# Kernel optimization log

Measured on AMD Instinct MI355X. Metric: run time of the kernel, lower is better.

Reference implementation:

```python
import jax, jax.numpy as jnp
import numpy as np

B, S, E = 4, 2048, 1024
H, DK, DV = 16, 64, 128


def setup_inputs() -> dict:
    key = jax.random.key(0)
    ks = jax.random.split(key, 9)
    scale = 0.02
    x = jax.random.normal(ks[0], (B, S, E), dtype=jnp.float32)
    # Per-head linear weights stacked along a head axis (same math as the
    # torch ModuleList of nn.Linear(embed_dim, d) layers).
    Wq = jax.random.normal(ks[1], (H, E, DK), dtype=jnp.float32) * scale
    bq = jax.random.normal(ks[2], (H, DK), dtype=jnp.float32) * scale
    Wk = jax.random.normal(ks[3], (H, E, DK), dtype=jnp.float32) * scale
    bk = jax.random.normal(ks[4], (H, DK), dtype=jnp.float32) * scale
    Wv = jax.random.normal(ks[5], (H, E, DV), dtype=jnp.float32) * scale
    bv = jax.random.normal(ks[6], (H, DV), dtype=jnp.float32) * scale
    Wo = jax.random.normal(ks[7], (H * DV, E), dtype=jnp.float32) * scale
    bo = jax.random.normal(ks[8], (E,), dtype=jnp.float32) * scale
    return {"x": x, "Wq": Wq, "bq": bq, "Wk": Wk, "bk": bk,
            "Wv": Wv, "bv": bv, "Wo": Wo, "bo": bo}


def reference(x, Wq, bq, Wk, bk, Wv, bv, Wo, bo):
    # Batched equivalent of the per-head Linear loop: [B,S,E] x [H,E,D] -> [B,H,S,D]
    Q = jnp.einsum('bse,hed->bhsd', x, Wq) + bq[None, :, None, :]
    K = jnp.einsum('bse,hed->bhsd', x, Wk) + bk[None, :, None, :]
    V = jnp.einsum('bse,hed->bhsd', x, Wv) + bv[None, :, None, :]
    scale = 1.0 / jnp.sqrt(jnp.asarray(Q.shape[-1], dtype=Q.dtype))
    scores = jnp.einsum('bhqd,bhkd->bhqk', Q, K) * scale  # [B,H,S,S]
    causal_mask = jnp.triu(jnp.ones((S, S), dtype=bool), k=1)  # True above diagonal
    scores = jnp.where(causal_mask[None, None], jnp.asarray(-jnp.inf, scores.dtype), scores)
    probs = jax.nn.softmax(scores, axis=-1)
    attn = jnp.einsum('bhqk,bhkd->bhqd', probs, V)  # [B,H,S,DV]
    # transpose(1,2).view(B,S,H*DV)
    concat = attn.transpose(0, 2, 1, 3).reshape(x.shape[0], x.shape[1], -1)
    return concat @ Wo + bo
```

## Files before the change

kernel.cpp:

```cpp
#include <hip/hip_runtime.h>

typedef __bf16 bf16x8 __attribute__((ext_vector_type(8)));
typedef float f32x4 __attribute__((ext_vector_type(4)));
typedef float f32x16 __attribute__((ext_vector_type(16)));

static constexpr int Bb = 4, Ss = 2048, Ee = 1024, Hh = 16, DKk = 64, DVv = 128;
static constexpr int Mm = Bb * Ss;
static constexpr int NQ = Hh * DKk;
static constexpr int NV = Hh * DVv;

#define MFMA16 __builtin_amdgcn_mfma_f32_16x16x32_bf16
#define MFMA32 __builtin_amdgcn_mfma_f32_32x32x16_bf16

#define GLL16(g, l) __builtin_amdgcn_global_load_lds(                        \
    (const __attribute__((address_space(1))) void*)(g),                      \
    (__attribute__((address_space(3))) void*)(l), 16, 0, 0)

#define SBAR()   asm volatile("s_barrier" ::: "memory")
#define WLGKM0() do { asm volatile("s_waitcnt lgkmcnt(0)" ::: "memory"); \
                      __builtin_amdgcn_sched_barrier(0); } while (0)
#define WVM(n)   asm volatile("s_waitcnt vmcnt(" #n ")" ::: "memory")

static __device__ __forceinline__ unsigned short f2b(float f) {
  unsigned int u = __float_as_uint(f);
  u += 0x7fffu + ((u >> 16) & 1u);
  return (unsigned short)(u >> 16);
}

__global__ __launch_bounds__(256) void cast_x_kernel(const float* __restrict__ in,
                                                     unsigned short* __restrict__ out, int n4) {
  int i = blockIdx.x * 256 + threadIdx.x;
  if (i >= n4) return;
  float4 v = reinterpret_cast<const float4*>(in)[i];
  ushort4 o;
  o.x = f2b(v.x); o.y = f2b(v.y); o.z = f2b(v.z); o.w = f2b(v.w);
  reinterpret_cast<ushort4*>(out)[i] = o;
}

__global__ __launch_bounds__(256) void transpose_cast_kernel(const float* __restrict__ in,
                                                             unsigned short* __restrict__ out,
                                                             int R, int C) {
  __shared__ float tile[32][33];
  int c0 = blockIdx.x * 32, r0 = blockIdx.y * 32;
  const float* ip = in + (size_t)blockIdx.z * R * C;
  unsigned short* op = out + (size_t)blockIdx.z * R * C;
  int tx = threadIdx.x, ty = threadIdx.y;
#pragma unroll
  for (int i = 0; i < 32; i += 8)
    tile[ty + i][tx] = ip[(size_t)(r0 + ty + i) * C + (c0 + tx)];
  __syncthreads();
#pragma unroll
  for (int i = 0; i < 32; i += 8)
    op[(size_t)(c0 + ty + i) * R + (r0 + tx)] = f2b(tile[tx][ty + i]);
}

template <int OUTMODE>
__global__ __launch_bounds__(512, 2) void gemm9_kernel(const unsigned short* __restrict__ A,
                                                       const unsigned short* __restrict__ BT,
                                                       const float* __restrict__ bias1,
                                                       const float* __restrict__ bias2,
                                                       void* __restrict__ out1,
                                                       void* __restrict__ out2,
                                                       int N, int K) {
  __shared__ unsigned short As0[256 * 64], As1[256 * 64];
  __shared__ unsigned short Bs0[256 * 64], Bs1[256 * 64];
  const int tid = threadIdx.x, wave = tid >> 6, lane = tid & 63;
  const int wm = wave >> 2, wn = wave & 3;
  const int l15 = lane & 15, lq = lane >> 4;
  const int nwg = gridDim.x, cpx = nwg >> 3;
  const int orig = (blockIdx.x & 7) * cpx + (blockIdx.x >> 3);
  const int bm = (orig & 31) << 8, bn = (orig >> 5) << 8;
  const int srow = tid >> 3;
  const int ssw = (((tid & 7) ^ (srow & 7)) << 3);
  const int rsw = l15 & 7;
  const int nIter = K >> 7;

  f32x4 acc[8][4] = {};
  bf16x8 bf[2][4];

#define LDA9(ASQ, MI, KK) \
  (*reinterpret_cast<const bf16x8*>(&(ASQ)[(size_t)((wm * 128 + (MI)*16 + l15) * 64) + (((((KK)*4 + lq)) ^ rsw) << 3)]))
#define LDB9(BSQ, NI, KK) \
  (*reinterpret_cast<const bf16x8*>(&(BSQ)[(size_t)((wn * 64 + (NI)*16 + l15) * 64) + (((((KK)*4 + lq)) ^ rsw) << 3)]))

  auto stA = [&](unsigned short* dst, int kt) {
#pragma unroll
    for (int k4 = 0; k4 < 4; ++k4)
      GLL16(A + (size_t)(bm + srow + k4 * 64) * K + kt * 64 + ssw,
            &dst[(size_t)(tid + k4 * 512) * 8]);
  };
  auto stB = [&](unsigned short* dst, int kt) {
#pragma unroll
    for (int k4 = 0; k4 < 4; ++k4)
      GLL16(BT + (size_t)(bn + srow + k4 * 64) * K + kt * 64 + ssw,
            &dst[(size_t)(tid + k4 * 512) * 8]);
  };

  stA(As0, 0);
  stB(Bs0, 0);
  stB(Bs1, 1);
  WVM(0);
  SBAR();

  for (int it = 0; it < nIter; ++it) {
    const bool notlast = (it < nIter - 1);
    {
      bf16x8 af[2][4];
#pragma unroll
      for (int kk = 0; kk < 2; ++kk)
#pragma unroll
        for (int m = 0; m < 4; ++m) af[kk][m] = LDA9(As0, m, kk);
#pragma unroll
      for (int kk = 0; kk < 2; ++kk)
#pragma unroll
        for (int ni = 0; ni < 4; ++ni) bf[kk][ni] = LDB9(Bs0, ni, kk);
      stA(As1, 2 * it + 1);
      SBAR();
      WLGKM0();
      __builtin_amdgcn_s_setprio(1);
#pragma unroll
      for (int kk = 0; kk < 2; ++kk)
#pragma unroll
        for (int m = 0; m < 4; ++m)
#pragma unroll
          for (int ni = 0; ni < 4; ++ni)
            acc[m][ni] = MFMA16(af[kk][m], bf[kk][ni], acc[m][ni], 0, 0, 0);
      __builtin_amdgcn_s_setprio(0);
      SBAR();
    }
    {
      bf16x8 af[2][4];
#pragma unroll
      for (int kk = 0; kk < 2; ++kk)
#pragma unroll
        for (int m = 0; m < 4; ++m) af[kk][m] = LDA9(As0, 4 + m, kk);
      if (notlast) stB(Bs0, 2 * it + 2);
      SBAR();
      WLGKM0();
      __builtin_amdgcn_s_setprio(1);
#pragma unroll
      for (int kk = 0; kk < 2; ++kk)
#pragma unroll
        for (int m = 0; m < 4; ++m)
#pragma unroll
          for (int ni = 0; ni < 4; ++ni)
            acc[4 + m][ni] = MFMA16(af[kk][m], bf[kk][ni], acc[4 + m][ni], 0, 0, 0);
      __builtin_amdgcn_s_setprio(0);
      if (notlast) { WVM(4); } else { WVM(0); }
      SBAR();
    }
    {
      bf16x8 af[2][4];
#pragma unroll
      for (int kk = 0; kk < 2; ++kk)
#pragma unroll
        for (int m = 0; m < 4; ++m) af[kk][m] = LDA9(As1, m, kk);
#pragma unroll
      for (int kk = 0; kk < 2; ++kk)
#pragma unroll
        for (int ni = 0; ni < 4; ++ni) bf[kk][ni] = LDB9(Bs1, ni, kk);
      if (notlast) stA(As0, 2 * it + 2);
      SBAR();
      WLGKM0();
      __builtin_amdgcn_s_setprio(1);
#pragma unroll
      for (int kk = 0; kk < 2; ++kk)
#pragma unroll
        for (int m = 0; m < 4; ++m)
#pragma unroll
          for (int ni = 0; ni < 4; ++ni)
            acc[m][ni] = MFMA16(af[kk][m], bf[kk][ni], acc[m][ni], 0, 0, 0);
      __builtin_amdgcn_s_setprio(0);
      SBAR();
    }
    {
      bf16x8 af[2][4];
#pragma unroll
      for (int kk = 0; kk < 2; ++kk)
#pragma unroll
        for (int m = 0; m < 4; ++m) af[kk][m] = LDA9(As1, 4 + m, kk);
      if (notlast) stB(Bs1, 2 * it + 3);
      SBAR();
      WLGKM0();
      __builtin_amdgcn_s_setprio(1);
#pragma unroll
      for (int kk = 0; kk < 2; ++kk)
#pragma unroll
        for (int m = 0; m < 4; ++m)
#pragma unroll
          for (int ni = 0; ni < 4; ++ni)
            acc[4 + m][ni] = MFMA16(af[kk][m], bf[kk][ni], acc[4 + m][ni], 0, 0, 0);
      __builtin_amdgcn_s_setprio(0);
      if (notlast) WVM(4);
      SBAR();
    }
  }

  const float SCLQ = 0.125f * 1.44269504088896f;
#pragma unroll
  for (int ni = 0; ni < 4; ++ni) {
    int col = bn + wn * 64 + ni * 16 + l15;
    float bs;
    if (OUTMODE == 4)
      bs = (col < 1024) ? bias1[col] : bias2[col - 1024];
    else
      bs = bias1[col];
#pragma unroll
    for (int mi = 0; mi < 8; ++mi) {
      int row0 = bm + wm * 128 + mi * 16 + (lq << 2);
      if (OUTMODE == 2) {
        int b_ = row0 >> 11, s0 = row0 & 2047;
        unsigned short* dst = (unsigned short*)out1 +
            ((size_t)((b_ * Hh + (col >> 7)) * DVv + (col & 127))) * Ss + s0;
        ushort4 o;
        o.x = f2b(acc[mi][ni][0] + bs);
        o.y = f2b(acc[mi][ni][1] + bs);
        o.z = f2b(acc[mi][ni][2] + bs);
        o.w = f2b(acc[mi][ni][3] + bs);
        *reinterpret_cast<ushort4*>(dst) = o;
      } else {
        unsigned short* tgt = (unsigned short*)(col < 1024 ? out1 : out2);
        int cc = col & 1023, hh = cc >> 6, d = cc & 63;
#pragma unroll
        for (int r = 0; r < 4; ++r) {
          int row = row0 + r;
          int b_ = row >> 11, s0 = row & 2047;
          float v = acc[mi][ni][r] + bs;
          if (col < 1024) v *= SCLQ;
          tgt[(((size_t)(b_ * Hh + hh) * Ss + s0) << 6) + d] = f2b(v);
        }
      }
    }
  }
#undef LDA9
#undef LDB9
}

__global__ __launch_bounds__(512, 2) void gemm8f_kernel(const unsigned short* __restrict__ A,
                                                        const unsigned short* __restrict__ BT,
                                                        const float* __restrict__ bias1,
                                                        float* __restrict__ out1,
                                                        int N, int K) {
  __shared__ unsigned short As0[256 * 64], As1[256 * 64];
  __shared__ unsigned short Bs0[128 * 64], Bs1[128 * 64];
  const int tid = threadIdx.x, wave = tid >> 6, lane = tid & 63;
  const int wm = wave >> 1, wn = wave & 1;
  const int l15 = lane & 15, lq = lane >> 4;
  const int nwg = gridDim.x, cpx = nwg >> 3;
  const int orig = (blockIdx.x & 7) * cpx + (blockIdx.x >> 3);
  const int bm = (orig & 31) << 8, bn = (orig >> 5) << 7;
  const int srow = tid >> 3;
  const int ssw = (((tid & 7) ^ (srow & 7)) << 3);
  const int rsw = l15 & 7;
  const int nIter = K >> 7;

  f32x4 acc[4][4] = {};
  bf16x8 bf[2][4];

#define LDA(ASQ, MI, KK) \
  (*reinterpret_cast<const bf16x8*>(&(ASQ)[(size_t)((wm * 64 + (MI)*16 + l15) * 64) + (((((KK)*4 + lq)) ^ rsw) << 3)]))
#define LDB(BSQ, NI, KK) \
  (*reinterpret_cast<const bf16x8*>(&(BSQ)[(size_t)((wn * 64 + (NI)*16 + l15) * 64) + (((((KK)*4 + lq)) ^ rsw) << 3)]))

  auto stA = [&](unsigned short* dst, int kt) {
#pragma unroll
    for (int k4 = 0; k4 < 4; ++k4)
      GLL16(A + (size_t)(bm + srow + k4 * 64) * K + kt * 64 + ssw,
            &dst[(size_t)(tid + k4 * 512) * 8]);
  };
  auto stB = [&](unsigned short* dst, int kt) {
#pragma unroll
    for (int k4 = 0; k4 < 2; ++k4)
      GLL16(BT + (size_t)(bn + srow + k4 * 64) * K + kt * 64 + ssw,
            &dst[(size_t)(tid + k4 * 512) * 8]);
  };

  stA(As0, 0);
  stB(Bs0, 0);
  stB(Bs1, 1);
  WVM(0);
  SBAR();

  for (int it = 0; it < nIter; ++it) {
    const bool notlast = (it < nIter - 1);
    {
      bf16x8 af[2][2];
      af[0][0] = LDA(As0, 0, 0); af[0][1] = LDA(As0, 1, 0);
      af[1][0] = LDA(As0, 0, 1); af[1][1] = LDA(As0, 1, 1);
#pragma unroll
      for (int kk = 0; kk < 2; ++kk)
#pragma unroll
        for (int ni = 0; ni < 4; ++ni) bf[kk][ni] = LDB(Bs0, ni, kk);
      stA(As1, 2 * it + 1);
      SBAR();
      WLGKM0();
      __builtin_amdgcn_s_setprio(1);
#pragma unroll
      for (int kk = 0; kk < 2; ++kk)
#pragma unroll
        for (int i = 0; i < 2; ++i)
#pragma unroll
          for (int ni = 0; ni < 4; ++ni)
            acc[i][ni] = MFMA16(af[kk][i], bf[kk][ni], acc[i][ni], 0, 0, 0);
      __builtin_amdgcn_s_setprio(0);
      SBAR();
    }
    {
      bf16x8 af[2][2];
      af[0][0] = LDA(As0, 2, 0); af[0][1] = LDA(As0, 3, 0);
      af[1][0] = LDA(As0, 2, 1); af[1][1] = LDA(As0, 3, 1);
      if (notlast) stB(Bs0, 2 * it + 2);
      SBAR();
      WLGKM0();
      __builtin_amdgcn_s_setprio(1);
#pragma unroll
      for (int kk = 0; kk < 2; ++kk)
#pragma unroll
        for (int i = 0; i < 2; ++i)
#pragma unroll
          for (int ni = 0; ni < 4; ++ni)
            acc[2 + i][ni] = MFMA16(af[kk][i], bf[kk][ni], acc[2 + i][ni], 0, 0, 0);
      __builtin_amdgcn_s_setprio(0);
      if (notlast) { WVM(2); } else { WVM(0); }
      SBAR();
    }
    {
      bf16x8 af[2][2];
      af[0][0] = LDA(As1, 0, 0); af[0][1] = LDA(As1, 1, 0);
      af[1][0] = LDA(As1, 0, 1); af[1][1] = LDA(As1, 1, 1);
#pragma unroll
      for (int kk = 0; kk < 2; ++kk)
#pragma unroll
        for (int ni = 0; ni < 4; ++ni) bf[kk][ni] = LDB(Bs1, ni, kk);
      if (notlast) stA(As0, 2 * it + 2);
      SBAR();
      WLGKM0();
      __builtin_amdgcn_s_setprio(1);
#pragma unroll
      for (int kk = 0; kk < 2; ++kk)
#pragma unroll
        for (int i = 0; i < 2; ++i)
#pragma unroll
          for (int ni = 0; ni < 4; ++ni)
            acc[i][ni] = MFMA16(af[kk][i], bf[kk][ni], acc[i][ni], 0, 0, 0);
      __builtin_amdgcn_s_setprio(0);
      SBAR();
    }
    {
      bf16x8 af[2][2];
      af[0][0] = LDA(As1, 2, 0); af[0][1] = LDA(As1, 3, 0);
      af[1][0] = LDA(As1, 2, 1); af[1][1] = LDA(As1, 3, 1);
      if (notlast) stB(Bs1, 2 * it + 3);
      SBAR();
      WLGKM0();
      __builtin_amdgcn_s_setprio(1);
#pragma unroll
      for (int kk = 0; kk < 2; ++kk)
#pragma unroll
        for (int i = 0; i < 2; ++i)
#pragma unroll
          for (int ni = 0; ni < 4; ++ni)
            acc[2 + i][ni] = MFMA16(af[kk][i], bf[kk][ni], acc[2 + i][ni], 0, 0, 0);
      __builtin_amdgcn_s_setprio(0);
      if (notlast) WVM(2);
      SBAR();
    }
  }

#pragma unroll
  for (int ni = 0; ni < 4; ++ni) {
    int col = bn + wn * 64 + ni * 16 + l15;
    float bs = bias1[col];
#pragma unroll
    for (int mi = 0; mi < 4; ++mi) {
      int row0 = bm + wm * 64 + mi * 16 + (lq << 2);
#pragma unroll
      for (int r = 0; r < 4; ++r)
        out1[(size_t)(row0 + r) * N + col] = acc[mi][ni][r] + bs;
    }
  }
#undef LDA
#undef LDB
}

__global__ __launch_bounds__(512, 1) void attn14_kernel(const unsigned short* __restrict__ Qh,
                                                        const unsigned short* __restrict__ Kh,
                                                        const unsigned short* __restrict__ Vt,
                                                        unsigned short* __restrict__ Aw) {
  __shared__ unsigned short Kb[2][128 * 64];
  __shared__ unsigned short Vb[2][128 * 128];
  const int bid = blockIdx.x;
  const int xcd = bid & 7, sub_ = bid >> 3;
  const int bhL = sub_ >> 2, q = sub_ & 3;
  const int bh = xcd + (bhL << 3);
  const int b = bh >> 4, h = bh & 15;
  const int tid = threadIdx.x, wave = tid >> 6, lane = tid & 63;
  const int l31 = lane & 31, lh = lane >> 5;

  const unsigned short* Qsrc = Qh + (size_t)(b * Hh + h) * Ss * DKk;
  const unsigned short* Ksrc = Kh + (size_t)(b * Hh + h) * Ss * DKk;
  const unsigned short* Vsrc = Vt + (size_t)(b * Hh + h) * (size_t)DVv * Ss;
  unsigned short* Adst = Aw + (size_t)b * Ss * NV + h * DVv;

  const int srowK = tid >> 3, schK = tid & 7;
  const int srowV = tid >> 4, schV = tid & 15;
  const int rx = l31 & 7;
  const int rxv = l31 & 15;

  union PU { unsigned u[4]; bf16x8 v; };

#pragma unroll 1
  for (int ph = 0; ph < 2; ++ph) {
    const int qt = ph ? q : 7 - q;
    const int nt2 = (qt + 1) * 2;
    const int q0w = qt * 256 + wave * 32;

    bf16x8 qf[4];
#pragma unroll
    for (int ks = 0; ks < 4; ++ks)
      qf[ks] = *reinterpret_cast<const bf16x8*>(
          Qsrc + (size_t)(q0w + l31) * DKk + ks * 16 + lh * 8);

    f32x16 accO[4] = {};
    float mrow = -1e30f, lrow = 0.f;

    {
#pragma unroll
      for (int k4 = 0; k4 < 2; ++k4) {
        int kvr = srowK + k4 * 64;
        GLL16(Ksrc + (size_t)kvr * DKk + ((schK ^ (kvr & 7)) << 3),
              &Kb[0][(size_t)(tid + k4 * 512) * 8]);
      }
#pragma unroll
      for (int k4 = 0; k4 < 4; ++k4) {
        int dvr = srowV + k4 * 32;
        GLL16(Vsrc + (size_t)dvr * Ss + ((schV ^ (dvr & 15)) << 3),
              &Vb[0][(size_t)(tid + k4 * 512) * 8]);
      }
    }

    for (int T = 0; T < nt2; ++T) {
      const int cur = T & 1;
      __syncthreads();
      if (T + 1 < nt2) {
        const int nb2 = (T + 1) * 128;
        const int nxt = cur ^ 1;
#pragma unroll
        for (int k4 = 0; k4 < 2; ++k4) {
          int kvr = srowK + k4 * 64;
          GLL16(Ksrc + (size_t)(nb2 + kvr) * DKk + ((schK ^ (kvr & 7)) << 3),
                &Kb[nxt][(size_t)(tid + k4 * 512) * 8]);
        }
#pragma unroll
        for (int k4 = 0; k4 < 4; ++k4) {
          int dvr = srowV + k4 * 32;
          GLL16(Vsrc + (size_t)dvr * Ss + nb2 + ((schV ^ (dvr & 15)) << 3),
                &Vb[nxt][(size_t)(tid + k4 * 512) * 8]);
        }
      }
#pragma unroll 1
      for (int sub = 0; sub < 2; ++sub) {
        const int kbase = T * 128 + sub * 64;
        if (kbase > q0w + 31) continue;

        f32x16 accS[2] = {};
        __builtin_amdgcn_s_setprio(1);
#pragma unroll
        for (int kvb = 0; kvb < 2; ++kvb)
#pragma unroll
          for (int ks = 0; ks < 4; ++ks) {
            const int row = sub * 64 + kvb * 32 + l31;
            bf16x8 kf = *reinterpret_cast<const bf16x8*>(
                &Kb[cur][row * 64 + (((ks * 2 + lh) ^ rx) << 3)]);
            accS[kvb] = MFMA32(kf, qf[ks], accS[kvb], 0, 0, 0);
          }
        __builtin_amdgcn_s_setprio(0);

        if (kbase + 63 > q0w) {
          int qg = q0w + l31;
#pragma unroll
          for (int kvb = 0; kvb < 2; ++kvb)
#pragma unroll
            for (int reg = 0; reg < 16; ++reg) {
              int kvg = kbase + kvb * 32 + (reg & 3) + 8 * (reg >> 2) + 4 * lh;
              if (kvg > qg) accS[kvb][reg] = -1e30f;
            }
        }
        float t[8];
#pragma unroll
        for (int i = 0; i < 8; ++i)
          t[i] = fmaxf(fmaxf(accS[0][i], accS[0][i + 8]), fmaxf(accS[1][i], accS[1][i + 8]));
        float pmx = fmaxf(fmaxf(fmaxf(t[0], t[1]), fmaxf(t[2], t[3])),
                          fmaxf(fmaxf(t[4], t[5]), fmaxf(t[6], t[7])));
        pmx = fmaxf(pmx, __shfl_xor(pmx, 32));
        float mn = mrow;
        if (!__all(pmx - mn <= 8.f)) {
          float mnew = fmaxf(mn, pmx);
          float al = exp2f(mn - mnew);
          mrow = mnew;
          lrow *= al;
#pragma unroll
          for (int reg = 0; reg < 16; ++reg) {
            float a = __shfl(al, (reg & 3) + 8 * (reg >> 2) + 4 * lh);
#pragma unroll
            for (int dvb = 0; dvb < 4; ++dvb) accO[dvb][reg] *= a;
          }
          mn = mnew;
        }
        float rs = 0.f;
#pragma unroll
        for (int kvb = 0; kvb < 2; ++kvb)
#pragma unroll
          for (int reg = 0; reg < 16; ++reg) {
            float e = exp2f(accS[kvb][reg] - mn);
            accS[kvb][reg] = e;
            rs += e;
          }
        rs += __shfl_xor(rs, 32);
        lrow += rs;
        bf16x8 pfrag[4];
#pragma unroll
        for (int kvb = 0; kvb < 2; ++kvb)
#pragma unroll
          for (int s = 0; s < 2; ++s) {
            const int B0 = s * 8;
            unsigned a, c, bb, d;
            asm("v_cvt_pk_bf16_f32 %0, %1, %2" : "=v"(a) : "v"(accS[kvb][B0 + 0]), "v"(accS[kvb][B0 + 1]));
            asm("v_cvt_pk_bf16_f32 %0, %1, %2" : "=v"(c) : "v"(accS[kvb][B0 + 2]), "v"(accS[kvb][B0 + 3]));
            asm("v_cvt_pk_bf16_f32 %0, %1, %2" : "=v"(bb) : "v"(accS[kvb][B0 + 4]), "v"(accS[kvb][B0 + 5]));
            asm("v_cvt_pk_bf16_f32 %0, %1, %2" : "=v"(d) : "v"(accS[kvb][B0 + 6]), "v"(accS[kvb][B0 + 7]));
            asm volatile("v_permlane32_swap_b32 %0, %1" : "+v"(a), "+v"(bb));
            asm volatile("v_permlane32_swap_b32 %0, %1" : "+v"(c), "+v"(d));
            PU u;
            u.u[0] = a; u.u[1] = c; u.u[2] = bb; u.u[3] = d;
            pfrag[kvb * 2 + s] = u.v;
          }
        __builtin_amdgcn_s_setprio(1);
#pragma unroll
        for (int dvb = 0; dvb < 4; ++dvb) {
          const int dv = dvb * 32 + l31;
          const unsigned short* vr = &Vb[cur][dv * 128];
#pragma unroll
          for (int ks = 0; ks < 4; ++ks) {
            bf16x8 vf = *reinterpret_cast<const bf16x8*>(
                vr + ((((sub << 3) + ks * 2 + lh) ^ rxv) << 3));
            accO[dvb] = MFMA32(pfrag[ks], vf, accO[dvb], 0, 0, 0);
          }
        }
        __builtin_amdgcn_s_setprio(0);
      }
    }
    float linv = 1.f / lrow;
#pragma unroll
    for (int reg = 0; reg < 16; ++reg) {
      int qr = (reg & 3) + 8 * (reg >> 2) + 4 * lh;
      float li = __shfl(linv, qr);
      int row = q0w + qr;
#pragma unroll
      for (int dvb = 0; dvb < 4; ++dvb)
        Adst[(size_t)row * NV + dvb * 32 + l31] = f2b(accO[dvb][reg] * li);
    }
    __syncthreads();
  }
}

extern "C" void kernel_launch(void* const* d_in, const int* in_sizes, int n_in,
                              void* d_out, int out_size, void* d_ws, size_t ws_size,
                              hipStream_t stream) {
  (void)in_sizes; (void)n_in; (void)out_size; (void)ws_size;
  const float* x  = (const float*)d_in[0];
  const float* Wq = (const float*)d_in[1];
  const float* bq = (const float*)d_in[2];
  const float* Wk = (const float*)d_in[3];
  const float* bk = (const float*)d_in[4];
  const float* Wv = (const float*)d_in[5];
  const float* bv = (const float*)d_in[6];
  const float* Wo = (const float*)d_in[7];
  const float* bo = (const float*)d_in[8];
  float* out = (float*)d_out;

  unsigned short* ws = (unsigned short*)d_ws;
  unsigned short* xb  = ws;
  unsigned short* WqT = xb  + 8388608;
  unsigned short* WkT = WqT + 1048576;
  unsigned short* WvT = WkT + 1048576;
  unsigned short* WoT = WvT + 2097152;
  unsigned short* Qw  = WoT + 2097152;
  unsigned short* Kw  = Qw  + 8388608;
  unsigned short* Vtw = Kw  + 8388608;
  unsigned short* Aw  = Vtw + 16777216;

  cast_x_kernel<<<dim3(8192), dim3(256), 0, stream>>>(x, xb, (Mm * Ee) / 4);

  transpose_cast_kernel<<<dim3(2, 32, 16), dim3(32, 8), 0, stream>>>(Wq, WqT, Ee, DKk);
  transpose_cast_kernel<<<dim3(2, 32, 16), dim3(32, 8), 0, stream>>>(Wk, WkT, Ee, DKk);
  transpose_cast_kernel<<<dim3(4, 32, 16), dim3(32, 8), 0, stream>>>(Wv, WvT, Ee, DVv);
  transpose_cast_kernel<<<dim3(32, 64, 1), dim3(32, 8), 0, stream>>>(Wo, WoT, NV, Ee);

  gemm9_kernel<4><<<dim3(256), dim3(512), 0, stream>>>(xb, WqT, bq, bk, Qw, Kw, 2048, Ee);
  gemm9_kernel<2><<<dim3(256), dim3(512), 0, stream>>>(xb, WvT, bv, nullptr, Vtw, nullptr, NV, Ee);

  attn14_kernel<<<dim3(256), dim3(512), 0, stream>>>(Qw, Kw, Vtw, Aw);

  gemm8f_kernel<<<dim3(256), dim3(512), 0, stream>>>(Aw, WoT, bo, out, NQ, NV);
}
```

Measured before the change: 246.6 us.

## Restructure GEMM mainloops into per-tile double-buffered prefetch; tree-reduce softmax row sums

```diff
diff --git a/kernel.cpp b/kernel.cpp
--- a/kernel.cpp
+++ b/kernel.cpp
@@ -55,13 +55,13 @@
 }
 
 template <int OUTMODE>
-__global__ __launch_bounds__(512, 2) void gemm9_kernel(const unsigned short* __restrict__ A,
-                                                       const unsigned short* __restrict__ BT,
-                                                       const float* __restrict__ bias1,
-                                                       const float* __restrict__ bias2,
-                                                       void* __restrict__ out1,
-                                                       void* __restrict__ out2,
-                                                       int N, int K) {
+__global__ __launch_bounds__(512, 2) void gemm10_kernel(const unsigned short* __restrict__ A,
+                                                        const unsigned short* __restrict__ BT,
+                                                        const float* __restrict__ bias1,
+                                                        const float* __restrict__ bias2,
+                                                        void* __restrict__ out1,
+                                                        void* __restrict__ out2,
+                                                        int N, int K) {
   __shared__ unsigned short As0[256 * 64], As1[256 * 64];
   __shared__ unsigned short Bs0[256 * 64], Bs1[256 * 64];
   const int tid = threadIdx.x, wave = tid >> 6, lane = tid & 63;
@@ -73,15 +73,14 @@
   const int srow = tid >> 3;
   const int ssw = (((tid & 7) ^ (srow & 7)) << 3);
   const int rsw = l15 & 7;
-  const int nIter = K >> 7;
+  const int nIter = K >> 6;
 
   f32x4 acc[8][4] = {};
-  bf16x8 bf[2][4];
-
-#define LDA9(ASQ, MI, KK) \
-  (*reinterpret_cast<const bf16x8*>(&(ASQ)[(size_t)((wm * 128 + (MI)*16 + l15) * 64) + (((((KK)*4 + lq)) ^ rsw) << 3)]))
-#define LDB9(BSQ, NI, KK) \
-  (*reinterpret_cast<const bf16x8*>(&(BSQ)[(size_t)((wn * 64 + (NI)*16 + l15) * 64) + (((((KK)*4 + lq)) ^ rsw) << 3)]))
+
+#define LDAx(P, MI, KK) \
+  (*reinterpret_cast<const bf16x8*>(&(P)[(size_t)((wm * 128 + (MI)*16 + l15) * 64) + (((((KK)*4 + lq)) ^ rsw) << 3)]))
+#define LDBx(P, NI, KK) \
+  (*reinterpret_cast<const bf16x8*>(&(P)[(size_t)((wn * 64 + (NI)*16 + l15) * 64) + (((((KK)*4 + lq)) ^ rsw) << 3)]))
 
   auto stA = [&](unsigned short* dst, int kt) {
 #pragma unroll
@@ -96,104 +95,58 @@
             &dst[(size_t)(tid + k4 * 512) * 8]);
   };
 
+  auto tile = [&](int t, unsigned short* Acur, unsigned short* Bcur,
+                  unsigned short* Anxt, unsigned short* Bnxt) {
+    SBAR();
+    if (t + 1 < nIter) {
+      stA(Anxt, t + 1);
+      stB(Bnxt, t + 1);
+      WVM(8);
+    } else {
+      WVM(0);
+    }
+    SBAR();
+    bf16x8 bfr[2][4], af[2][4];
+#pragma unroll
+    for (int kk = 0; kk < 2; ++kk)
+#pragma unroll
+      for (int ni = 0; ni < 4; ++ni) bfr[kk][ni] = LDBx(Bcur, ni, kk);
+#pragma unroll
+    for (int kk = 0; kk < 2; ++kk)
+#pragma unroll
+      for (int m = 0; m < 4; ++m) af[kk][m] = LDAx(Acur, m, kk);
+    WLGKM0();
+    __builtin_amdgcn_s_setprio(1);
+#pragma unroll
+    for (int kk = 0; kk < 2; ++kk)
+#pragma unroll
+      for (int m = 0; m < 4; ++m)
+#pragma unroll
+        for (int ni = 0; ni < 4; ++ni)
+          acc[m][ni] = MFMA16(af[kk][m], bfr[kk][ni], acc[m][ni], 0, 0, 0);
+    __builtin_amdgcn_s_setprio(0);
+#pragma unroll
+    for (int kk = 0; kk < 2; ++kk)
+#pragma unroll
+      for (int m = 0; m < 4; ++m) af[kk][m] = LDAx(Acur, 4 + m, kk);
+    WLGKM0();
+    __builtin_amdgcn_s_setprio(1);
+#pragma unroll
+    for (int kk = 0; kk < 2; ++kk)
+#pragma unroll
+      for (int m = 0; m < 4; ++m)
+#pragma unroll
+        for (int ni = 0; ni < 4; ++ni)
+          acc[4 + m][ni] = MFMA16(af[kk][m], bfr[kk][ni], acc[4 + m][ni], 0, 0, 0);
+    __builtin_amdgcn_s_setprio(0);
+  };
+
   stA(As0, 0);
   stB(Bs0, 0);
-  stB(Bs1, 1);
-  WVM(0);
-  SBAR();
-
-  for (int it = 0; it < nIter; ++it) {
-    const bool notlast = (it < nIter - 1);
-    {
-      bf16x8 af[2][4];
-#pragma unroll
-      for (int kk = 0; kk < 2; ++kk)
-#pragma unroll
-        for (int m = 0; m < 4; ++m) af[kk][m] = LDA9(As0, m, kk);
-#pragma unroll
-      for (int kk = 0; kk < 2; ++kk)
-#pragma unroll
-        for (int ni = 0; ni < 4; ++ni) bf[kk][ni] = LDB9(Bs0, ni, kk);
-      stA(As1, 2 * it + 1);
-      SBAR();
-      WLGKM0();
-      __builtin_amdgcn_s_setprio(1);
-#pragma unroll
-      for (int kk = 0; kk < 2; ++kk)
-#pragma unroll
-        for (int m = 0; m < 4; ++m)
-#pragma unroll
-          for (int ni = 0; ni < 4; ++ni)
-            acc[m][ni] = MFMA16(af[kk][m], bf[kk][ni], acc[m][ni], 0, 0, 0);
-      __builtin_amdgcn_s_setprio(0);
-      SBAR();
-    }
-    {
-      bf16x8 af[2][4];
-#pragma unroll
-      for (int kk = 0; kk < 2; ++kk)
-#pragma unroll
-        for (int m = 0; m < 4; ++m) af[kk][m] = LDA9(As0, 4 + m, kk);
-      if (notlast) stB(Bs0, 2 * it + 2);
-      SBAR();
-      WLGKM0();
-      __builtin_amdgcn_s_setprio(1);
-#pragma unroll
-      for (int kk = 0; kk < 2; ++kk)
-#pragma unroll
-        for (int m = 0; m < 4; ++m)
-#pragma unroll
-          for (int ni = 0; ni < 4; ++ni)
-            acc[4 + m][ni] = MFMA16(af[kk][m], bf[kk][ni], acc[4 + m][ni], 0, 0, 0);
-      __builtin_amdgcn_s_setprio(0);
-      if (notlast) { WVM(4); } else { WVM(0); }
-      SBAR();
-    }
-    {
-      bf16x8 af[2][4];
-#pragma unroll
-      for (int kk = 0; kk < 2; ++kk)
-#pragma unroll
-        for (int m = 0; m < 4; ++m) af[kk][m] = LDA9(As1, m, kk);
-#pragma unroll
-      for (int kk = 0; kk < 2; ++kk)
-#pragma unroll
-        for (int ni = 0; ni < 4; ++ni) bf[kk][ni] = LDB9(Bs1, ni, kk);
-      if (notlast) stA(As0, 2 * it + 2);
-      SBAR();
-      WLGKM0();
-      __builtin_amdgcn_s_setprio(1);
-#pragma unroll
-      for (int kk = 0; kk < 2; ++kk)
-#pragma unroll
-        for (int m = 0; m < 4; ++m)
-#pragma unroll
-          for (int ni = 0; ni < 4; ++ni)
-            acc[m][ni] = MFMA16(af[kk][m], bf[kk][ni], acc[m][ni], 0, 0, 0);
-      __builtin_amdgcn_s_setprio(0);
-      SBAR();
-    }
-    {
-      bf16x8 af[2][4];
-#pragma unroll
-      for (int kk = 0; kk < 2; ++kk)
-#pragma unroll
-        for (int m = 0; m < 4; ++m) af[kk][m] = LDA9(As1, 4 + m, kk);
-      if (notlast) stB(Bs1, 2 * it + 3);
-      SBAR();
-      WLGKM0();
-      __builtin_amdgcn_s_setprio(1);
-#pragma unroll
-      for (int kk = 0; kk < 2; ++kk)
-#pragma unroll
-        for (int m = 0; m < 4; ++m)
-#pragma unroll
-          for (int ni = 0; ni < 4; ++ni)
-            acc[4 + m][ni] = MFMA16(af[kk][m], bf[kk][ni], acc[4 + m][ni], 0, 0, 0);
-      __builtin_amdgcn_s_setprio(0);
-      if (notlast) WVM(4);
-      SBAR();
-    }
+
+  for (int it = 0; it < nIter; it += 2) {
+    tile(it, As0, Bs0, As1, Bs1);
+    tile(it + 1, As1, Bs1, As0, Bs0);
   }
 
   const float SCLQ = 0.125f * 1.44269504088896f;
@@ -232,15 +185,15 @@
       }
     }
   }
-#undef LDA9
-#undef LDB9
-}
-
-__global__ __launch_bounds__(512, 2) void gemm8f_kernel(const unsigned short* __restrict__ A,
-                                                        const unsigned short* __restrict__ BT,
-                                                        const float* __restrict__ bias1,
-                                                        float* __restrict__ out1,
-                                                        int N, int K) {
+#undef LDAx
+#undef LDBx
+}
+
+__global__ __launch_bounds__(512, 2) void gemm10f_kernel(const unsigned short* __restrict__ A,
+                                                         const unsigned short* __restrict__ BT,
+                                                         const float* __restrict__ bias1,
+                                                         float* __restrict__ out1,
+                                                         int N, int K) {
   __shared__ unsigned short As0[256 * 64], As1[256 * 64];
   __shared__ unsigned short Bs0[128 * 64], Bs1[128 * 64];
   const int tid = threadIdx.x, wave = tid >> 6, lane = tid & 63;
@@ -252,15 +205,14 @@
   const int srow = tid >> 3;
   const int ssw = (((tid & 7) ^ (srow & 7)) << 3);
   const int rsw = l15 & 7;
-  const int nIter = K >> 7;
+  const int nIter = K >> 6;
 
   f32x4 acc[4][4] = {};
-  bf16x8 bf[2][4];
-
-#define LDA(ASQ, MI, KK) \
-  (*reinterpret_cast<const bf16x8*>(&(ASQ)[(size_t)((wm * 64 + (MI)*16 + l15) * 64) + (((((KK)*4 + lq)) ^ rsw) << 3)]))
-#define LDB(BSQ, NI, KK) \
-  (*reinterpret_cast<const bf16x8*>(&(BSQ)[(size_t)((wn * 64 + (NI)*16 + l15) * 64) + (((((KK)*4 + lq)) ^ rsw) << 3)]))
+
+#define LDAf(P, MI, KK) \
+  (*reinterpret_cast<const bf16x8*>(&(P)[(size_t)((wm * 64 + (MI)*16 + l15) * 64) + (((((KK)*4 + lq)) ^ rsw) << 3)]))
+#define LDBf(P, NI, KK) \
+  (*reinterpret_cast<const bf16x8*>(&(P)[(size_t)((wn * 64 + (NI)*16 + l15) * 64) + (((((KK)*4 + lq)) ^ rsw) << 3)]))
 
   auto stA = [&](unsigned short* dst, int kt) {
 #pragma unroll
@@ -275,96 +227,44 @@
             &dst[(size_t)(tid + k4 * 512) * 8]);
   };
 
+  auto tile = [&](int t, unsigned short* Acur, unsigned short* Bcur,
+                  unsigned short* Anxt, unsigned short* Bnxt) {
+    SBAR();
+    if (t + 1 < nIter) {
+      stA(Anxt, t + 1);
+      stB(Bnxt, t + 1);
+      WVM(6);
+    } else {
+      WVM(0);
+    }
+    SBAR();
+    bf16x8 bfr[2][4], af[2][4];
+#pragma unroll
+    for (int kk = 0; kk < 2; ++kk)
+#pragma unroll
+      for (int ni = 0; ni < 4; ++ni) bfr[kk][ni] = LDBf(Bcur, ni, kk);
+#pragma unroll
+    for (int kk = 0; kk < 2; ++kk)
+#pragma unroll
+      for (int m = 0; m < 4; ++m) af[kk][m] = LDAf(Acur, m, kk);
+    WLGKM0();
+    __builtin_amdgcn_s_setprio(1);
+#pragma unroll
+    for (int kk = 0; kk < 2; ++kk)
+#pragma unroll
+      for (int m = 0; m < 4; ++m)
+#pragma unroll
+        for (int ni = 0; ni < 4; ++ni)
+          acc[m][ni] = MFMA16(af[kk][m], bfr[kk][ni], acc[m][ni], 0, 0, 0);
+    __builtin_amdgcn_s_setprio(0);
+  };
+
   stA(As0, 0);
   stB(Bs0, 0);
-  stB(Bs1, 1);
-  WVM(0);
-  SBAR();
-
-  for (int it = 0; it < nIter; ++it) {
-    const bool notlast = (it < nIter - 1);
-    {
-      bf16x8 af[2][2];
-      af[0][0] = LDA(As0, 0, 0); af[0][1] = LDA(As0, 1, 0);
-      af[1][0] = LDA(As0, 0, 1); af[1][1] = LDA(As0, 1, 1);
-#pragma unroll
-      for (int kk = 0; kk < 2; ++kk)
-#pragma unroll
-        for (int ni = 0; ni < 4; ++ni) bf[kk][ni] = LDB(Bs0, ni, kk);
-      stA(As1, 2 * it + 1);
-      SBAR();
-      WLGKM0();
-      __builtin_amdgcn_s_setprio(1);
-#pragma unroll
-      for (int kk = 0; kk < 2; ++kk)
-#pragma unroll
-        for (int i = 0; i < 2; ++i)
-#pragma unroll
-          for (int ni = 0; ni < 4; ++ni)
-            acc[i][ni] = MFMA16(af[kk][i], bf[kk][ni], acc[i][ni], 0, 0, 0);
-      __builtin_amdgcn_s_setprio(0);
-      SBAR();
-    }
-    {
-      bf16x8 af[2][2];
-      af[0][0] = LDA(As0, 2, 0); af[0][1] = LDA(As0, 3, 0);
-      af[1][0] = LDA(As0, 2, 1); af[1][1] = LDA(As0, 3, 1);
-      if (notlast) stB(Bs0, 2 * it + 2);
-      SBAR();
-      WLGKM0();
-      __builtin_amdgcn_s_setprio(1);
-#pragma unroll
-      for (int kk = 0; kk < 2; ++kk)
-#pragma unroll
-        for (int i = 0; i < 2; ++i)
-#pragma unroll
-          for (int ni = 0; ni < 4; ++ni)
-            acc[2 + i][ni] = MFMA16(af[kk][i], bf[kk][ni], acc[2 + i][ni], 0, 0, 0);
-      __builtin_amdgcn_s_setprio(0);
-      if (notlast) { WVM(2); } else { WVM(0); }
-      SBAR();
-    }
-    {
-      bf16x8 af[2][2];
-      af[0][0] = LDA(As1, 0, 0); af[0][1] = LDA(As1, 1, 0);
-      af[1][0] = LDA(As1, 0, 1); af[1][1] = LDA(As1, 1, 1);
-#pragma unroll
-      for (int kk = 0; kk < 2; ++kk)
-#pragma unroll
-        for (int ni = 0; ni < 4; ++ni) bf[kk][ni] = LDB(Bs1, ni, kk);
-      if (notlast) stA(As0, 2 * it + 2);
-      SBAR();
-      WLGKM0();
-      __builtin_amdgcn_s_setprio(1);
-#pragma unroll
-      for (int kk = 0; kk < 2; ++kk)
-#pragma unroll
-        for (int i = 0; i < 2; ++i)
-#pragma unroll
-          for (int ni = 0; ni < 4; ++ni)
-            acc[i][ni] = MFMA16(af[kk][i], bf[kk][ni], acc[i][ni], 0, 0, 0);
-      __builtin_amdgcn_s_setprio(0);
-      SBAR();
-    }
-    {
-      bf16x8 af[2][2];
-      af[0][0] = LDA(As1, 2, 0); af[0][1] = LDA(As1, 3, 0);
-      af[1][0] = LDA(As1, 2, 1); af[1][1] = LDA(As1, 3, 1);
-      if (notlast) stB(Bs1, 2 * it + 3);
-      SBAR();
-      WLGKM0();
-      __builtin_amdgcn_s_setprio(1);
-#pragma unroll
-      for (int kk = 0; kk < 2; ++kk)
-#pragma unroll
-        for (int i = 0; i < 2; ++i)
-#pragma unroll
-          for (int ni = 0; ni < 4; ++ni)
-            acc[2 + i][ni] = MFMA16(af[kk][i], bf[kk][ni], acc[2 + i][ni], 0, 0, 0);
-      __builtin_amdgcn_s_setprio(0);
-      if (notlast) WVM(2);
-      SBAR();
-    }
+
+  for (int it = 0; it < nIter; it += 2) {
+    tile(it, As0, Bs0, As1, Bs1);
+    tile(it + 1, As1, Bs1, As0, Bs0);
   }
 
 #pragma unroll
@@ -379,11 +279,11 @@
         out1[(size_t)(row0 + r) * N + col] = acc[mi][ni][r] + bs;
     }
   }
-#undef LDA
-#undef LDB
-}
-
-__global__ __launch_bounds__(512, 1) void attn14_kernel(const unsigned short* __restrict__ Qh,
+#undef LDAf
+#undef LDBf
+}
+
+__global__ __launch_bounds__(512, 1) void attn15_kernel(const unsigned short* __restrict__ Qh,
                                                         const unsigned short* __restrict__ Kh,
                                                         const unsigned short* __restrict__ Vt,
                                                         unsigned short* __restrict__ Aw) {
@@ -507,17 +407,22 @@
           }
           mn = mnew;
         }
-        float rs = 0.f;
 #pragma unroll
         for (int kvb = 0; kvb < 2; ++kvb)
 #pragma unroll
-          for (int reg = 0; reg < 16; ++reg) {
-            float e = exp2f(accS[kvb][reg] - mn);
-            accS[kvb][reg] = e;
-            rs += e;
-          }
-        rs += __shfl_xor(rs, 32);
-        lrow += rs;
+          for (int reg = 0; reg < 16; ++reg)
+            accS[kvb][reg] = exp2f(accS[kvb][reg] - mn);
+        {
+          f32x16 sv = accS[0] + accS[1];
+          float s8[8];
+#pragma unroll
+          for (int i = 0; i < 8; ++i) s8[i] = sv[i] + sv[i + 8];
+          float s40 = s8[0] + s8[4], s41 = s8[1] + s8[5];
+          float s42 = s8[2] + s8[6], s43 = s8[3] + s8[7];
+          float rs = (s40 + s41) + (s42 + s43);
+          rs += __shfl_xor(rs, 32);
+          lrow += rs;
+        }
         bf16x8 pfrag[4];
 #pragma unroll
         for (int kvb = 0; kvb < 2; ++kvb)
@@ -597,10 +502,10 @@
   transpose_cast_kernel<<<dim3(4, 32, 16), dim3(32, 8), 0, stream>>>(Wv, WvT, Ee, DVv);
   transpose_cast_kernel<<<dim3(32, 64, 1), dim3(32, 8), 0, stream>>>(Wo, WoT, NV, Ee);
 
-  gemm9_kernel<4><<<dim3(256), dim3(512), 0, stream>>>(xb, WqT, bq, bk, Qw, Kw, 2048, Ee);
-  gemm9_kernel<2><<<dim3(256), dim3(512), 0, stream>>>(xb, WvT, bv, nullptr, Vtw, nullptr, NV, Ee);
-
-  attn14_kernel<<<dim3(256), dim3(512), 0, stream>>>(Qw, Kw, Vtw, Aw);
-
-  gemm8f_kernel<<<dim3(256), dim3(512), 0, stream>>>(Aw, WoT, bo, out, NQ, NV);
-}
+  gemm10_kernel<4><<<dim3(256), dim3(512), 0, stream>>>(xb, WqT, bq, bk, Qw, Kw, 2048, Ee);
+  gemm10_kernel<2><<<dim3(256), dim3(512), 0, stream>>>(xb, WvT, bv, nullptr, Vtw, nullptr, NV, Ee);
+
+  attn15_kernel<<<dim3(256), dim3(512), 0, stream>>>(Qw, Kw, Vtw, Aw);
+
+  gemm10f_kernel<<<dim3(256), dim3(512), 0, stream>>>(Aw, WoT, bo, out, NQ, NV);
+}
```

Measured after the change: 253.8 us. 2.9% more time.
